# Performance work log

Hardware: AMD Instinct MI355X
Metric: run time of the kernel (lower is better)

## Reference

```python
import jax, jax.numpy as jnp
import numpy as np

B, S, D = 4, 2048, 1024
D_K, D_V = 1024, 1024


def setup_inputs() -> dict:
    key = jax.random.key(0)
    ks = jax.random.split(key, 9)
    s = 1.0 / np.sqrt(D)
    return {
        "q_in": jax.random.normal(ks[0], (B, S, D), jnp.float32),
        "k_in": jax.random.normal(ks[1], (B, S, D), jnp.float32),
        "v_in": jax.random.normal(ks[2], (B, S, D), jnp.float32),
        "Wq": jax.random.normal(ks[3], (D, D_K), jnp.float32) * s,
        "bq": jnp.zeros((D_K,), jnp.float32),
        "Wk": jax.random.normal(ks[4], (D, D_K), jnp.float32) * s,
        "bk": jnp.zeros((D_K,), jnp.float32),
        "Wv": jax.random.normal(ks[5], (D, D_V), jnp.float32) * s,
        "bv": jnp.zeros((D_V,), jnp.float32),
    }


def reference(q_in, k_in, v_in, Wq, bq, Wk, bk, Wv, bv):
    q = jnp.einsum("bsd,dk->bsk", q_in, Wq) + bq  # [B,S,d_k]
    k = jnp.einsum("bsd,dk->bsk", k_in, Wk) + bk  # [B,S,d_k]
    v = jnp.einsum("bsd,dv->bsv", v_in, Wv) + bv  # [B,S,d_v]
    scores = jnp.einsum("bqk,bsk->bqs", q, k) / jnp.sqrt(jnp.float32(D_K))
    attn = jax.nn.softmax(scores, axis=-1)  # [B,S,S]
    return jnp.einsum("bqs,bsv->bqv", attn, v)
```

## Files before the change

kernel.cpp:

```cpp
#include <hip/hip_runtime.h>
#include <stdint.h>

#define B_  4
#define S_  2048
#define D_  1024
#define DK_ 1024
#define DV_ 1024

typedef __attribute__((ext_vector_type(8)))  short short8;
typedef __attribute__((ext_vector_type(16))) float floatx16;

#define ASYNC16(gsrc, ldst)                                                        \
  __builtin_amdgcn_global_load_lds(                                                \
      (const __attribute__((address_space(1))) unsigned int*)(gsrc),               \
      (__attribute__((address_space(3))) unsigned int*)(ldst), 16, 0, 0)

#define WAITVM(N) asm volatile("s_waitcnt vmcnt(" #N ")" ::: "memory")

__device__ __forceinline__ unsigned short f2bf(float f) {
  union { float f; uint32_t u; } v; v.f = f;
  uint32_t r = v.u + 0x7fffu + ((v.u >> 16) & 1u);
  return (unsigned short)(r >> 16);
}

__global__ __launch_bounds__(256)
void prep(const float* __restrict__ q, const float* __restrict__ k, const float* __restrict__ v,
          const float* __restrict__ W0, const float* __restrict__ W1, const float* __restrict__ W2,
          unsigned short* __restrict__ qkv, unsigned short* __restrict__ WT) {
  const int bid = blockIdx.x, tid = threadIdx.x;
  if (bid < 12288) {
    const int t  = bid >> 12;
    const int cb = bid & 4095;
    const float* in = (t == 0) ? q : (t == 1) ? k : v;
    unsigned short* o = qkv + (long)t * ((long)B_ * S_ * D_);
    const int i0 = cb * 512 + tid;
    float4 v0 = ((const float4*)in)[i0];
    float4 v1 = ((const float4*)in)[i0 + 256];
    ushort4 u0, u1;
    u0.x = f2bf(v0.x); u0.y = f2bf(v0.y); u0.z = f2bf(v0.z); u0.w = f2bf(v0.w);
    u1.x = f2bf(v1.x); u1.y = f2bf(v1.y); u1.z = f2bf(v1.z); u1.w = f2bf(v1.w);
    ((ushort4*)o)[i0] = u0;
    ((ushort4*)o)[i0 + 256] = u1;
  } else {
    const int b2 = bid - 12288;
    const int w  = b2 >> 10;
    const int tl = b2 & 1023;
    const float* in = (w == 0) ? W0 : (w == 1) ? W1 : W2;
    unsigned short* o = WT + (long)w * D_ * DK_;
    __shared__ float tile[32][33];
    const int bx = (tl & 31) * 32, by = (tl >> 5) * 32;
    const int tx = tid & 31, ty = tid >> 5;
    for (int r = ty; r < 32; r += 8)
      tile[r][tx] = in[(long)(by + r) * DK_ + bx + tx];
    __syncthreads();
    for (int r = ty; r < 32; r += 8)
      o[(long)(bx + r) * D_ + by + tx] = f2bf(tile[tx][r]);
  }
}

__device__ __forceinline__ void storeC(float* p, float v)          { *p = v; }
__device__ __forceinline__ void storeC(unsigned short* p, float v) { *p = f2bf(v); }

template <typename OutT, int NOUT, int MODE, int KSPL>
__global__ __launch_bounds__(512, 2)
void gemm_bt256(const unsigned short* __restrict__ A0, const unsigned short* __restrict__ A1,
                const unsigned short* __restrict__ A2, const unsigned short* __restrict__ Bm,
                OutT* __restrict__ C0, OutT* __restrict__ C1, OutT* __restrict__ C2,
                const float* __restrict__ b0, const float* __restrict__ b1,
                const float* __restrict__ b2, float* __restrict__ rowsum,
                int N, int K, int lda, int ldb, long sA, long sB, long sC, float scale) {
  __shared__ __align__(16) unsigned short As[3][256 * 32];
  __shared__ __align__(16) unsigned short Bs[3][256 * 32];
  __shared__ float invs[256];
  const int tid  = threadIdx.x;
  const int lane = tid & 63, wave = tid >> 6;
  const int wm = (wave >> 2) * 128;
  const int wn = (wave & 3) * 64;
  const int lm = lane & 31;
  const int hi = lane >> 5;

  const int gx = gridDim.x, gy = gridDim.y;
  const int T  = gx * gy * (int)gridDim.z;
  const int l  = blockIdx.x + gx * (blockIdx.y + gy * blockIdx.z);
  const int l2 = (l & 7) * (T >> 3) + (l >> 3);
  const int bxi = l2 % gx;
  const int byi = (l2 / gx) % gy;
  const int bzi = l2 / (gx * gy);

  const int  kh = (KSPL > 1) ? (bzi & (KSPL - 1)) : 0;
  const long zb = (KSPL > 1) ? (bzi >> 1) : bzi;
  const int m0  = byi * 256;
  const int n0g = bxi * 256;

  const unsigned short* A = A0;
  OutT* C = C0;
  const float* bias = b0;
  int n0 = n0g, sel = 0;
  if (NOUT == 3) {
    sel = n0g >> 10;
    n0 = n0g & 1023;
    if (sel == 1)      { A = A1; C = C1; bias = b1; }
    else if (sel == 2) { A = A2; C = C2; bias = b2; }
  }
  A += zb * sA + (long)kh * K;
  const unsigned short* Bp = Bm + zb * sB + (long)kh * K;
  C += zb * sC;

  const int rr = lane >> 2;
  const int cc = (((lane & 3) ^ ((lane >> 3) & 3)) * 8);
  const unsigned short* gA0 = A  + (long)(m0  + 16 * wave + rr) * lda + cc;
  const unsigned short* gA1 = gA0 + 128 * (long)lda;
  const unsigned short* gB0 = Bp + (long)(n0g + 16 * wave + rr) * ldb + cc;
  const unsigned short* gB1 = gB0 + 128 * (long)ldb;
  const int la0 = wave * 512, la1 = (wave + 8) * 512;

  floatx16 acc[4][2] = {};
  const int sw = (lm >> 1) & 3;

#define GEMM_COMPUTE(pp)                                                                \
  _Pragma("unroll")                                                                     \
  for (int s = 0; s < 2; s++) {                                                         \
    const int off = ((s * 2 + hi) ^ sw) * 8;                                            \
    short8 af[4], bf[2];                                                                \
    _Pragma("unroll")                                                                   \
    for (int i = 0; i < 4; i++)                                                         \
      af[i] = *(const short8*)&As[pp][(wm + i * 32 + lm) * 32 + off];                   \
    _Pragma("unroll")                                                                   \
    for (int j = 0; j < 2; j++)                                                         \
      bf[j] = *(const short8*)&Bs[pp][(wn + j * 32 + lm) * 32 + off];                   \
    _Pragma("unroll")                                                                   \
    for (int i = 0; i < 4; i++)                                                         \
      _Pragma("unroll")                                                                 \
      for (int j = 0; j < 2; j++)                                                       \
        acc[i][j] = __builtin_amdgcn_mfma_f32_32x32x16_bf16(af[i], bf[j], acc[i][j], 0, 0, 0); \
  }

  ASYNC16(gA0, &As[0][la0]); ASYNC16(gA1, &As[0][la1]);
  ASYNC16(gB0, &Bs[0][la0]); ASYNC16(gB1, &Bs[0][la1]);
  gA0 += 32; gA1 += 32; gB0 += 32; gB1 += 32;
  ASYNC16(gA0, &As[1][la0]); ASYNC16(gA1, &As[1][la1]);
  ASYNC16(gB0, &Bs[1][la0]); ASYNC16(gB1, &Bs[1][la1]);
  gA0 += 32; gA1 += 32; gB0 += 32; gB1 += 32;

  const int nk = K >> 5;
  int pc = 0, pn = 2;
  for (int kt = 0; kt < nk - 1; kt++) {
    WAITVM(4);
    __builtin_amdgcn_s_barrier();
    if (kt + 2 < nk) {
      ASYNC16(gA0, &As[pn][la0]); ASYNC16(gA1, &As[pn][la1]);
      ASYNC16(gB0, &Bs[pn][la0]); ASYNC16(gB1, &Bs[pn][la1]);
      gA0 += 32; gA1 += 32; gB0 += 32; gB1 += 32;
    }
    GEMM_COMPUTE(pc)
    pc = (pc == 2) ? 0 : pc + 1;
    pn = (pn == 2) ? 0 : pn + 1;
  }
  WAITVM(0);
  __builtin_amdgcn_s_barrier();
  GEMM_COMPUTE(pc)

  if (MODE == 2 || MODE == 3) {
    __syncthreads();
    if (tid < 256) invs[tid] = 1.0f / rowsum[zb * S_ + m0 + tid];
    __syncthreads();
  }

  if (NOUT == 3 && sel == 2) {
    unsigned short* Vt = (unsigned short*)C;
    const int b = m0 >> 11;
    const int sbase = (m0 & 2047);
#pragma unroll
    for (int i = 0; i < 4; i++) {
      const int srowb = sbase + wm + i * 32 + (hi << 2);
#pragma unroll
      for (int j = 0; j < 2; j++) {
        const int col = n0 + wn + j * 32 + lm;
        const float bv = bias[col];
        unsigned short* vp = Vt + ((long)b * DV_ + col) * S_ + srowb;
#pragma unroll
        for (int g = 0; g < 4; g++) {
          ushort4 u;
          u.x = f2bf(acc[i][j][4 * g + 0] + bv);
          u.y = f2bf(acc[i][j][4 * g + 1] + bv);
          u.z = f2bf(acc[i][j][4 * g + 2] + bv);
          u.w = f2bf(acc[i][j][4 * g + 3] + bv);
          *(ushort4*)(vp + 8 * g) = u;
        }
      }
    }
  } else if (MODE == 1) {
#pragma unroll
    for (int i = 0; i < 4; i++) {
#pragma unroll
      for (int r = 0; r < 16; r++) {
        const int row = m0 + wm + i * 32 + (r & 3) + ((r >> 2) << 3) + (hi << 2);
        float sum2 = 0.f;
#pragma unroll
        for (int j = 0; j < 2; j++) {
          const int col = n0 + wn + j * 32 + lm;
          float e = __expf(acc[i][j][r] * scale);
          storeC(C + (long)row * N + col, e);
          sum2 += e;
        }
#pragma unroll
        for (int msk = 1; msk < 32; msk <<= 1) sum2 += __shfl_xor(sum2, msk, 64);
        if ((lane & 31) == 0) atomicAdd(&rowsum[zb * S_ + row], sum2);
      }
    }
  } else {
#pragma unroll
    for (int i = 0; i < 4; i++) {
#pragma unroll
      for (int j = 0; j < 2; j++) {
        const int col = n0 + wn + j * 32 + lm;
        const float bv = bias ? bias[col] : 0.f;
#pragma unroll
        for (int r = 0; r < 16; r++) {
          const int rl = wm + i * 32 + (r & 3) + ((r >> 2) << 3) + (hi << 2);
          float val = acc[i][j][r] * scale + bv;
          if (MODE == 3) {
            atomicAdd((float*)(C + (long)(m0 + rl) * N + col), val * invs[rl]);
          } else {
            if (MODE == 2) val *= invs[rl];
            storeC(C + (long)(m0 + rl) * N + col, val);
          }
        }
      }
    }
  }
#undef GEMM_COMPUTE
}

extern "C" void kernel_launch(void* const* d_in, const int* in_sizes, int n_in,
                              void* d_out, int out_size, void* d_ws, size_t ws_size,
                              hipStream_t stream) {
  const float* q_in = (const float*)d_in[0];
  const float* k_in = (const float*)d_in[1];
  const float* v_in = (const float*)d_in[2];
  const float* Wq   = (const float*)d_in[3];
  const float* bq   = (const float*)d_in[4];
  const float* Wk   = (const float*)d_in[5];
  const float* bk   = (const float*)d_in[6];
  const float* Wv   = (const float*)d_in[7];
  const float* bv   = (const float*)d_in[8];
  float* out = (float*)d_out;

  char* ws = (char*)d_ws;
  const long nX = (long)B_ * S_ * D_;
  const long nW = (long)D_ * DK_;
  unsigned short* qb  = (unsigned short*)(ws);
  unsigned short* kb  = qb + nX;
  unsigned short* vb  = kb + nX;
  unsigned short* WqT = vb + nX;
  unsigned short* Qb  = WqT + 3 * nW;
  unsigned short* Kb  = Qb + nX;
  unsigned short* Vt  = Kb + nX;
  float*          rowsum = (float*)(Vt + nX);
  unsigned short* U   = (unsigned short*)ws;

  dim3 blk(256), blk5(512);

  hipMemsetAsync(rowsum, 0, (size_t)B_ * S_ * sizeof(float), stream);
  hipMemsetAsync(out, 0, (size_t)B_ * S_ * DV_ * sizeof(float), stream);

  {
    dim3 g(12288 + 3072);
    prep<<<g, blk, 0, stream>>>(q_in, k_in, v_in, Wq, Wk, Wv, qb, WqT);
  }
  {
    dim3 g(3 * DK_ / 256, (B_ * S_) / 256, 1);
    gemm_bt256<unsigned short, 3, 0, 1><<<g, blk5, 0, stream>>>(
        qb, kb, vb, WqT, Qb, Kb, Vt, bq, bk, bv, nullptr,
        DK_, D_, D_, D_, 0, 0, 0, 1.f);
  }
  {
    dim3 g(S_ / 256, S_ / 256, B_);
    gemm_bt256<unsigned short, 1, 1, 1><<<g, blk5, 0, stream>>>(
        Qb, nullptr, nullptr, Kb, U, nullptr, nullptr, nullptr, nullptr, nullptr, rowsum,
        S_, DK_, DK_, DK_, (long)S_ * DK_, (long)S_ * DK_, (long)S_ * S_, 0.03125f);
  }
  {
    dim3 g(DV_ / 256, S_ / 256, B_ * 2);
    gemm_bt256<float, 1, 3, 2><<<g, blk5, 0, stream>>>(
        U, nullptr, nullptr, Vt, out, nullptr, nullptr, nullptr, nullptr, nullptr, rowsum,
        DV_, S_ / 2, S_, S_, (long)S_ * S_, (long)DV_ * S_, (long)S_ * DV_, 1.f);
  }
}
```

Baseline: 390.2 us.

## Restructure GEMM mainloop to double-buffered BK=64 with interleaved loads and setprio

Replaces the triple-buffered BK=32 LDS pipeline with a double-buffered BK=64 pipeline. Each tile is split into four compute quarters, and the next tile's A and B async loads are issued within the first two quarters. Barriers around MFMA clusters and s_setprio are meant to coordinate the waves and overlap the global loads with the matrix math. The change also adds more barriers per tile and doubles the LDS per buffer, which could reduce latency hiding or occupancy.

```diff
diff --git a/kernel.cpp b/kernel.cpp
--- a/kernel.cpp
+++ b/kernel.cpp
@@ -69,8 +69,8 @@
                 const float* __restrict__ b0, const float* __restrict__ b1,
                 const float* __restrict__ b2, float* __restrict__ rowsum,
                 int N, int K, int lda, int ldb, long sA, long sB, long sC, float scale) {
-  __shared__ __align__(16) unsigned short As[3][256 * 32];
-  __shared__ __align__(16) unsigned short Bs[3][256 * 32];
+  __shared__ __align__(16) unsigned short As[2][256 * 64];
+  __shared__ __align__(16) unsigned short Bs[2][256 * 64];
   __shared__ float invs[256];
   const int tid  = threadIdx.x;
   const int lane = tid & 63, wave = tid >> 6;
@@ -106,59 +106,70 @@
   const unsigned short* Bp = Bm + zb * sB + (long)kh * K;
   C += zb * sC;
 
-  const int rr = lane >> 2;
-  const int cc = (((lane & 3) ^ ((lane >> 3) & 3)) * 8);
-  const unsigned short* gA0 = A  + (long)(m0  + 16 * wave + rr) * lda + cc;
-  const unsigned short* gA1 = gA0 + 128 * (long)lda;
-  const unsigned short* gB0 = Bp + (long)(n0g + 16 * wave + rr) * ldb + cc;
-  const unsigned short* gB1 = gB0 + 128 * (long)ldb;
-  const int la0 = wave * 512, la1 = (wave + 8) * 512;
+  const int srow  = lane >> 3;
+  const int sslot = ((lane & 7) ^ srow) * 8;
+  const unsigned short* gA = A  + (long)(m0  + 32 * wave + srow) * lda + sslot;
+  const unsigned short* gB = Bp + (long)(n0g + 32 * wave + srow) * ldb + sslot;
+  const int lb = wave * 2048;
 
   floatx16 acc[4][2] = {};
-  const int sw = (lm >> 1) & 3;
-
-#define GEMM_COMPUTE(pp)                                                                \
-  _Pragma("unroll")                                                                     \
-  for (int s = 0; s < 2; s++) {                                                         \
-    const int off = ((s * 2 + hi) ^ sw) * 8;                                            \
-    short8 af[4], bf[2];                                                                \
-    _Pragma("unroll")                                                                   \
-    for (int i = 0; i < 4; i++)                                                         \
-      af[i] = *(const short8*)&As[pp][(wm + i * 32 + lm) * 32 + off];                   \
-    _Pragma("unroll")                                                                   \
-    for (int j = 0; j < 2; j++)                                                         \
-      bf[j] = *(const short8*)&Bs[pp][(wn + j * 32 + lm) * 32 + off];                   \
-    _Pragma("unroll")                                                                   \
-    for (int i = 0; i < 4; i++)                                                         \
-      _Pragma("unroll")                                                                 \
-      for (int j = 0; j < 2; j++)                                                       \
-        acc[i][j] = __builtin_amdgcn_mfma_f32_32x32x16_bf16(af[i], bf[j], acc[i][j], 0, 0, 0); \
-  }
-
-  ASYNC16(gA0, &As[0][la0]); ASYNC16(gA1, &As[0][la1]);
-  ASYNC16(gB0, &Bs[0][la0]); ASYNC16(gB1, &Bs[0][la1]);
-  gA0 += 32; gA1 += 32; gB0 += 32; gB1 += 32;
-  ASYNC16(gA0, &As[1][la0]); ASYNC16(gA1, &As[1][la1]);
-  ASYNC16(gB0, &Bs[1][la0]); ASYNC16(gB1, &Bs[1][la1]);
-  gA0 += 32; gA1 += 32; gB0 += 32; gB1 += 32;
-
-  const int nk = K >> 5;
-  int pc = 0, pn = 2;
-  for (int kt = 0; kt < nk - 1; kt++) {
-    WAITVM(4);
-    __builtin_amdgcn_s_barrier();
-    if (kt + 2 < nk) {
-      ASYNC16(gA0, &As[pn][la0]); ASYNC16(gA1, &As[pn][la1]);
-      ASYNC16(gB0, &Bs[pn][la0]); ASYNC16(gB1, &Bs[pn][la1]);
-      gA0 += 32; gA1 += 32; gB0 += 32; gB1 += 32;
-    }
-    GEMM_COMPUTE(pc)
-    pc = (pc == 2) ? 0 : pc + 1;
-    pn = (pn == 2) ? 0 : pn + 1;
-  }
+  const int swz = lm & 7;
+
+  const int nt = K >> 6;
+
+#pragma unroll
+  for (int a = 0; a < 4; a++) ASYNC16(gA + (long)(8 * a) * lda, &As[0][lb + a * 512]);
+#pragma unroll
+  for (int a = 0; a < 4; a++) ASYNC16(gB + (long)(8 * a) * ldb, &Bs[0][lb + a * 512]);
+  gA += 64; gB += 64;
   WAITVM(0);
   __builtin_amdgcn_s_barrier();
-  GEMM_COMPUTE(pc)
+
+  for (int t = 0; t < nt; t++) {
+    const int p = t & 1;
+    const bool pre = (t + 1 < nt);
+#pragma unroll
+    for (int q = 0; q < 4; q++) {
+      const int i0 = (q >> 1) * 2;
+      const int s0 = (q & 1) * 2;
+      short8 af[2][2], bf[2][2];
+#pragma unroll
+      for (int i = 0; i < 2; i++)
+#pragma unroll
+        for (int s = 0; s < 2; s++)
+          af[i][s] = *(const short8*)
+            &As[p][(wm + (i0 + i) * 32 + lm) * 64 + ((((s0 + s) * 2 + hi) ^ swz) * 8)];
+#pragma unroll
+      for (int j = 0; j < 2; j++)
+#pragma unroll
+        for (int s = 0; s < 2; s++)
+          bf[j][s] = *(const short8*)
+            &Bs[p][(wn + j * 32 + lm) * 64 + ((((s0 + s) * 2 + hi) ^ swz) * 8)];
+      if (q == 0 && pre) {
+#pragma unroll
+        for (int a = 0; a < 4; a++) ASYNC16(gA + (long)(8 * a) * lda, &As[p ^ 1][lb + a * 512]);
+      }
+      if (q == 1 && pre) {
+#pragma unroll
+        for (int a = 0; a < 4; a++) ASYNC16(gB + (long)(8 * a) * ldb, &Bs[p ^ 1][lb + a * 512]);
+        gA += 64; gB += 64;
+      }
+      __builtin_amdgcn_s_barrier();
+      asm volatile("s_waitcnt lgkmcnt(0)" ::: "memory");
+      __builtin_amdgcn_s_setprio(1);
+#pragma unroll
+      for (int s = 0; s < 2; s++)
+#pragma unroll
+        for (int i = 0; i < 2; i++)
+#pragma unroll
+          for (int j = 0; j < 2; j++)
+            acc[i0 + i][j] =
+                __builtin_amdgcn_mfma_f32_32x32x16_bf16(af[i][s], bf[j][s], acc[i0 + i][j], 0, 0, 0);
+      __builtin_amdgcn_s_setprio(0);
+      if (q == 3) WAITVM(0);
+      __builtin_amdgcn_s_barrier();
+    }
+  }
 
   if (MODE == 2 || MODE == 3) {
     __syncthreads();
@@ -229,7 +240,6 @@
       }
     }
   }
-#undef GEMM_COMPUTE
 }
 
 extern "C" void kernel_launch(void* const* d_in, const int* in_sizes, int n_in,
```

Measured after the change: 377.2 us. 1.03x faster.
